# Performance work log

Hardware: AMD Instinct MI355X
Metric: run time of the kernel (lower is better)

Reference implementation:

```python
import jax, jax.numpy as jnp
import numpy as np

N_NODES = 100000
N_EDGES = 1600000


def spmm(edge_index, edge_vals, x, n_nodes):
    # adj @ x with adj in COO form: out[dst] += val * x[src]
    src = edge_index[0]
    dst = edge_index[1]
    gathered = x[src] * edge_vals[:, None]  # [E, F]
    return jax.ops.segment_sum(gathered, dst, num_segments=n_nodes)


def setup_inputs() -> dict:
    key = jax.random.key(0)
    ks = jax.random.split(key, 8)
    x = jax.random.normal(ks[0], (N_NODES, 512), dtype=jnp.float32)
    edge_index = jax.random.randint(ks[1], (2, N_EDGES), 0, N_NODES, dtype=jnp.int64)
    edge_vals = jax.random.uniform(ks[2], (N_EDGES,), dtype=jnp.float32)
    # xavier-uniform style weights, zero biases (as in initialize_weights)
    def xavier(k, fan_in, fan_out):
        lim = float(np.sqrt(6.0 / (fan_in + fan_out)))
        return jax.random.uniform(k, (fan_in, fan_out), minval=-lim, maxval=lim, dtype=jnp.float32)
    W1 = xavier(ks[3], 512, 128)
    b1 = jnp.zeros((128,), jnp.float32)
    W2 = xavier(ks[4], 128, 64)
    b2 = jnp.zeros((64,), jnp.float32)
    W3 = xavier(ks[5], 64, 16)
    b3 = jnp.zeros((16,), jnp.float32)
    return {"x": x, "edge_index": edge_index, "edge_vals": edge_vals,
            "W1": W1, "b1": b1, "W2": W2, "b2": b2, "W3": W3, "b3": b3}


def reference(x, edge_index, edge_vals, W1, b1, W2, b2, W3, b3):
    n = x.shape[0]
    h = jax.nn.relu(spmm(edge_index, edge_vals, x @ W1 + b1, n))
    h = jax.nn.relu(spmm(edge_index, edge_vals, h @ W2 + b2, n))
    logits = spmm(edge_index, edge_vals, h @ W3 + b3, n)
    logp = jax.nn.log_softmax(logits, axis=1)
    return jnp.argmax(logp, axis=1)
```

## Files before the change

### kernel.cpp

```cpp
#include <hip/hip_runtime.h>

typedef _Float16 half8 __attribute__((ext_vector_type(8)));
typedef float floatx4 __attribute__((ext_vector_type(4)));

__device__ __forceinline__ void g2lds16(const void* g, void* l) {
    __builtin_amdgcn_global_load_lds(
        (const __attribute__((address_space(1))) void*)(unsigned long long)g,
        (__attribute__((address_space(3))) void*)(unsigned int)(unsigned long long)l,
        16, 0, 0);
}


__global__ __launch_bounds__(256) void hist_kernel(const int* __restrict__ dst,
                                                   int* __restrict__ count, int E) {
    int e = blockIdx.x * 256 + threadIdx.x;
    if (e < E) atomicAdd(&count[dst[e]], 1);
}

__global__ __launch_bounds__(1024) void scan_a(const int* __restrict__ count,
                                               int* __restrict__ incl,
                                               int* __restrict__ bsum, int N) {
    __shared__ int s[1024];
    int tid = threadIdx.x;
    int i = blockIdx.x * 1024 + tid;
    int v = (i < N) ? count[i] : 0;
    s[tid] = v;
    __syncthreads();
    for (int off = 1; off < 1024; off <<= 1) {
        int t = (tid >= off) ? s[tid - off] : 0;
        __syncthreads();
        s[tid] += t;
        __syncthreads();
    }
    if (i < N) incl[i] = s[tid];
    if (tid == 1023) bsum[blockIdx.x] = s[1023];
}

__global__ void scan_b(const int* __restrict__ bsum, int* __restrict__ boff, int NB) {
    if (threadIdx.x == 0 && blockIdx.x == 0) {
        int run = 0;
        for (int b = 0; b < NB; ++b) { int c = bsum[b]; boff[b] = run; run += c; }
    }
}

__global__ __launch_bounds__(1024) void scan_c(const int* __restrict__ count,
                                               const int* __restrict__ incl,
                                               const int* __restrict__ boff,
                                               int* __restrict__ rowptr,
                                               int* __restrict__ cursor, int N) {
    int i = blockIdx.x * 1024 + threadIdx.x;
    if (i < N) {
        int excl = incl[i] - count[i] + boff[blockIdx.x];
        rowptr[i] = excl;
        cursor[i] = excl;
        if (i == N - 1) rowptr[N] = incl[i] + boff[blockIdx.x];
    }
}

__global__ __launch_bounds__(256) void scatter_kernel(const int* __restrict__ src,
                                                      const int* __restrict__ dst,
                                                      const float* __restrict__ val,
                                                      int* __restrict__ cursor,
                                                      int* __restrict__ ssrc,
                                                      float* __restrict__ sval, int E) {
    int e = blockIdx.x * 256 + threadIdx.x;
    if (e < E) {
        int d = dst[e];
        int pos = atomicAdd(&cursor[d], 1);
        ssrc[pos] = src[e];
        sval[pos] = val[e];
    }
}


__global__ __launch_bounds__(256) void prep_w1(const float* __restrict__ W1,
                                               _Float16* __restrict__ Whi,
                                               _Float16* __restrict__ Wlo) {
    int tid = blockIdx.x * 256 + threadIdx.x;
    int n = tid >> 9;
    int k = tid & 511;
    float w = W1[(size_t)k * 128 + n];
    _Float16 h = (_Float16)w;
    Whi[tid] = h;
    Wlo[tid] = (_Float16)(w - (float)h);
}

__global__ __launch_bounds__(256) void prep_w2(const float* __restrict__ W2,
                                               _Float16* __restrict__ Whi,
                                               _Float16* __restrict__ Wlo) {
    int tid = blockIdx.x * 256 + threadIdx.x;
    int n = tid >> 7;
    int k = tid & 127;
    float w = W2[(size_t)k * 64 + n];
    _Float16 h = (_Float16)w;
    Whi[tid] = h;
    Wlo[tid] = (_Float16)(w - (float)h);
}

__device__ __forceinline__ void split8(float4 f0, float4 f1, half8& h, half8& l) {
    float f[8] = {f0.x, f0.y, f0.z, f0.w, f1.x, f1.y, f1.z, f1.w};
#pragma unroll
    for (int j = 0; j < 8; ++j) {
        _Float16 hi = (_Float16)f[j];
        h[j] = hi;
        l[j] = (_Float16)(f[j] - (float)hi);
    }
}


__global__ __launch_bounds__(256) void gemm1_mfma(const float* __restrict__ X,
                                                  const _Float16* __restrict__ Whi,
                                                  const _Float16* __restrict__ Wlo,
                                                  const float* __restrict__ bias,
                                                  float* __restrict__ out, int M) {
    __shared__ char smem[2 * 16384];
    int t = threadIdx.x;
    int w = t >> 6;
    int lane = t & 63;
    int quad = lane >> 4;
    int l16 = lane & 15;
    int bm = blockIdx.x * 128;
    int m0 = bm + w * 32;

    int ra0 = min(m0 + l16, M - 1);
    int ra1 = min(m0 + 16 + l16, M - 1);
    const float* a0p = X + (size_t)ra0 * 512 + quad * 8;
    const float* a1p = X + (size_t)ra1 * 512 + quad * 8;

    int chunk0 = w * 4;
    const _Float16* gsrc[4];
#pragma unroll
    for (int c = 0; c < 4; ++c) {
        int idx = (chunk0 + c) * 1024 + lane * 16;
        int sec = idx >> 13;
        int row = (idx & 8191) >> 6;
        int kch = (idx >> 4) & 3;
        gsrc[c] = (sec ? Wlo : Whi) + (size_t)row * 512 + kch * 8;
    }
#pragma unroll
    for (int c = 0; c < 4; ++c)
        g2lds16(gsrc[c], smem + (chunk0 + c) * 1024);

    floatx4 acc[2][8];
#pragma unroll
    for (int mt = 0; mt < 2; ++mt)
#pragma unroll
        for (int nt = 0; nt < 8; ++nt) acc[mt][nt] = (floatx4){0.f, 0.f, 0.f, 0.f};

    for (int i = 0; i < 16; ++i) {
        int k0 = i * 32;
        __syncthreads();
        float4 af00 = *(const float4*)(a0p + k0);
        float4 af01 = *(const float4*)(a0p + k0 + 4);
        float4 af10 = *(const float4*)(a1p + k0);
        float4 af11 = *(const float4*)(a1p + k0 + 4);
        if (i < 15) {
            char* nbuf = smem + ((i + 1) & 1) * 16384;
#pragma unroll
            for (int c = 0; c < 4; ++c)
                g2lds16(gsrc[c] + k0 + 32, nbuf + (chunk0 + c) * 1024);
        }
        const char* buf = smem + (i & 1) * 16384;
        half8 bh[8], bl[8];
#pragma unroll
        for (int nt = 0; nt < 8; ++nt) {
            int off = (nt * 16 + l16) * 64 + quad * 16;
            bh[nt] = *(const half8*)(buf + off);
            bl[nt] = *(const half8*)(buf + 8192 + off);
        }
        half8 ah0, al0, ah1, al1;
        split8(af00, af01, ah0, al0);
        split8(af10, af11, ah1, al1);
#pragma unroll
        for (int nt = 0; nt < 8; ++nt) {
            acc[0][nt] = __builtin_amdgcn_mfma_f32_16x16x32_f16(ah0, bh[nt], acc[0][nt], 0, 0, 0);
            acc[1][nt] = __builtin_amdgcn_mfma_f32_16x16x32_f16(ah1, bh[nt], acc[1][nt], 0, 0, 0);
            acc[0][nt] = __builtin_amdgcn_mfma_f32_16x16x32_f16(ah0, bl[nt], acc[0][nt], 0, 0, 0);
            acc[1][nt] = __builtin_amdgcn_mfma_f32_16x16x32_f16(ah1, bl[nt], acc[1][nt], 0, 0, 0);
            acc[0][nt] = __builtin_amdgcn_mfma_f32_16x16x32_f16(al0, bh[nt], acc[0][nt], 0, 0, 0);
            acc[1][nt] = __builtin_amdgcn_mfma_f32_16x16x32_f16(al1, bh[nt], acc[1][nt], 0, 0, 0);
        }
    }

#pragma unroll
    for (int nt = 0; nt < 8; ++nt) {
        int col = nt * 16 + l16;
        float bv = bias[col];
#pragma unroll
        for (int mt = 0; mt < 2; ++mt)
#pragma unroll
            for (int r = 0; r < 4; ++r) {
                int row = m0 + mt * 16 + quad * 4 + r;
                if (row < M) out[(size_t)row * 128 + col] = acc[mt][nt][r] + bv;
            }
    }
}


__global__ __launch_bounds__(256) void gemm2_mfma(const float* __restrict__ H,
                                                  const _Float16* __restrict__ Whi,
                                                  const _Float16* __restrict__ Wlo,
                                                  const float* __restrict__ bias,
                                                  float* __restrict__ out, int M) {
    __shared__ char smem[2 * 64 * 320];
    int t = threadIdx.x;
#pragma unroll
    for (int i = 0; i < 4; ++i) {
        int gidx = i * 256 + t;
        int row = gidx >> 4, col = gidx & 15;
        *(float4*)(smem + row * 320 + col * 16) = ((const float4*)Whi)[gidx];
        *(float4*)(smem + 20480 + row * 320 + col * 16) = ((const float4*)Wlo)[gidx];
    }
    __syncthreads();

    int w = t >> 6;
    int lane = t & 63;
    int quad = lane >> 4;
    int l16 = lane & 15;
    int m0 = blockIdx.x * 128 + w * 32;
    int ra0 = min(m0 + l16, M - 1);
    int ra1 = min(m0 + 16 + l16, M - 1);
    const float* a0p = H + (size_t)ra0 * 128 + quad * 8;
    const float* a1p = H + (size_t)ra1 * 128 + quad * 8;

    floatx4 acc[2][4];
#pragma unroll
    for (int mt = 0; mt < 2; ++mt)
#pragma unroll
        for (int nt = 0; nt < 4; ++nt) acc[mt][nt] = (floatx4){0.f, 0.f, 0.f, 0.f};

#pragma unroll
    for (int k0 = 0; k0 < 128; k0 += 32) {
        float4 af00 = *(const float4*)(a0p + k0);
        float4 af01 = *(const float4*)(a0p + k0 + 4);
        float4 af10 = *(const float4*)(a1p + k0);
        float4 af11 = *(const float4*)(a1p + k0 + 4);
        af00.x = fmaxf(af00.x, 0.f); af00.y = fmaxf(af00.y, 0.f);
        af00.z = fmaxf(af00.z, 0.f); af00.w = fmaxf(af00.w, 0.f);
        af01.x = fmaxf(af01.x, 0.f); af01.y = fmaxf(af01.y, 0.f);
        af01.z = fmaxf(af01.z, 0.f); af01.w = fmaxf(af01.w, 0.f);
        af10.x = fmaxf(af10.x, 0.f); af10.y = fmaxf(af10.y, 0.f);
        af10.z = fmaxf(af10.z, 0.f); af10.w = fmaxf(af10.w, 0.f);
        af11.x = fmaxf(af11.x, 0.f); af11.y = fmaxf(af11.y, 0.f);
        af11.z = fmaxf(af11.z, 0.f); af11.w = fmaxf(af11.w, 0.f);
        half8 bh[4], bl[4];
#pragma unroll
        for (int nt = 0; nt < 4; ++nt) {
            int off = (nt * 16 + l16) * 320 + k0 * 2 + quad * 16;
            bh[nt] = *(const half8*)(smem + off);
            bl[nt] = *(const half8*)(smem + 20480 + off);
        }
        half8 ah0, al0, ah1, al1;
        split8(af00, af01, ah0, al0);
        split8(af10, af11, ah1, al1);
#pragma unroll
        for (int nt = 0; nt < 4; ++nt) {
            acc[0][nt] = __builtin_amdgcn_mfma_f32_16x16x32_f16(ah0, bh[nt], acc[0][nt], 0, 0, 0);
            acc[1][nt] = __builtin_amdgcn_mfma_f32_16x16x32_f16(ah1, bh[nt], acc[1][nt], 0, 0, 0);
            acc[0][nt] = __builtin_amdgcn_mfma_f32_16x16x32_f16(ah0, bl[nt], acc[0][nt], 0, 0, 0);
            acc[1][nt] = __builtin_amdgcn_mfma_f32_16x16x32_f16(ah1, bl[nt], acc[1][nt], 0, 0, 0);
            acc[0][nt] = __builtin_amdgcn_mfma_f32_16x16x32_f16(al0, bh[nt], acc[0][nt], 0, 0, 0);
            acc[1][nt] = __builtin_amdgcn_mfma_f32_16x16x32_f16(al1, bh[nt], acc[1][nt], 0, 0, 0);
        }
    }

#pragma unroll
    for (int nt = 0; nt < 4; ++nt) {
        int col = nt * 16 + l16;
        float bv = bias[col];
#pragma unroll
        for (int mt = 0; mt < 2; ++mt)
#pragma unroll
            for (int r = 0; r < 4; ++r) {
                int row = m0 + mt * 16 + quad * 4 + r;
                if (row < M) out[(size_t)row * 64 + col] = acc[mt][nt][r] + bv;
            }
    }
}


__global__ __launch_bounds__(256) void gemm3(const float* __restrict__ H,
                                             const float* __restrict__ W,
                                             const float* __restrict__ bias,
                                             float* __restrict__ out, int M) {
    __shared__ float Ws[64 * 16];
    __shared__ float Xs[32 * 68];
    int t = threadIdx.x;
    int m0 = blockIdx.x * 32;
    ((float4*)Ws)[t] = ((const float4*)W)[t];
#pragma unroll
    for (int i = 0; i < 2; i++) {
        int idx = t + i * 256;
        int gi = idx * 4;
        int row = gi >> 6, col = gi & 63;
        float4 v = make_float4(0.f, 0.f, 0.f, 0.f);
        if (m0 + row < M) v = *(const float4*)(H + (size_t)(m0 + row) * 64 + col);
        v.x = fmaxf(v.x, 0.f); v.y = fmaxf(v.y, 0.f);
        v.z = fmaxf(v.z, 0.f); v.w = fmaxf(v.w, 0.f);
        *(float4*)&Xs[row * 68 + col] = v;
    }
    __syncthreads();
    int node = t >> 3;
    int j = t & 7;
    float a0 = 0.f, a1 = 0.f;
#pragma unroll 8
    for (int k = 0; k < 64; ++k) {
        float xv = Xs[node * 68 + k];
        a0 += xv * Ws[k * 16 + j * 2];
        a1 += xv * Ws[k * 16 + j * 2 + 1];
    }
    int row = m0 + node;
    if (row < M) {
        a0 += bias[j * 2];
        a1 += bias[j * 2 + 1];
        float2 r = make_float2(a0, a1);
        *(float2*)(out + (size_t)row * 16 + j * 2) = r;
    }
}


__global__ __launch_bounds__(256) void spmm128(const int* __restrict__ rowptr,
                                               const int* __restrict__ ssrc,
                                               const float* __restrict__ sval,
                                               const float* __restrict__ T,
                                               float* __restrict__ H, int N) {
    int lane = threadIdx.x & 63;
    int node = __builtin_amdgcn_readfirstlane(blockIdx.x * 4 + (threadIdx.x >> 6));
    if (node >= N) return;
    int beg = rowptr[node], end = rowptr[node + 1];
    float a0 = 0.f, a1 = 0.f;
    int i = beg;
    int n4 = beg + ((end - beg) & ~3);
    for (; i < n4; i += 4) {
        int s0 = ssrc[i], s1 = ssrc[i + 1], s2 = ssrc[i + 2], s3 = ssrc[i + 3];
        float v0 = sval[i], v1 = sval[i + 1], v2 = sval[i + 2], v3 = sval[i + 3];
        const float* p0 = T + (size_t)s0 * 128;
        const float* p1 = T + (size_t)s1 * 128;
        const float* p2 = T + (size_t)s2 * 128;
        const float* p3 = T + (size_t)s3 * 128;
        float x0 = p0[lane], y0 = p0[lane + 64];
        float x1 = p1[lane], y1 = p1[lane + 64];
        float x2 = p2[lane], y2 = p2[lane + 64];
        float x3 = p3[lane], y3 = p3[lane + 64];
        a0 += v0 * x0; a1 += v0 * y0;
        a0 += v1 * x1; a1 += v1 * y1;
        a0 += v2 * x2; a1 += v2 * y2;
        a0 += v3 * x3; a1 += v3 * y3;
    }
    for (; i < end; ++i) {
        int s = ssrc[i];
        float v = sval[i];
        const float* p = T + (size_t)s * 128;
        a0 += v * p[lane];
        a1 += v * p[lane + 64];
    }
    float* o = H + (size_t)node * 128;
    o[lane] = a0;
    o[lane + 64] = a1;
}

__global__ __launch_bounds__(256) void spmm64(const int* __restrict__ rowptr,
                                              const int* __restrict__ ssrc,
                                              const float* __restrict__ sval,
                                              const float* __restrict__ T,
                                              float* __restrict__ H, int N) {
    int lane = threadIdx.x & 63;
    int node = __builtin_amdgcn_readfirstlane(blockIdx.x * 4 + (threadIdx.x >> 6));
    if (node >= N) return;
    int beg = rowptr[node], end = rowptr[node + 1];
    float a = 0.f;
    int i = beg;
    int n4 = beg + ((end - beg) & ~3);
    for (; i < n4; i += 4) {
        int s0 = ssrc[i], s1 = ssrc[i + 1], s2 = ssrc[i + 2], s3 = ssrc[i + 3];
        float v0 = sval[i], v1 = sval[i + 1], v2 = sval[i + 2], v3 = sval[i + 3];
        float x0 = T[(size_t)s0 * 64 + lane];
        float x1 = T[(size_t)s1 * 64 + lane];
        float x2 = T[(size_t)s2 * 64 + lane];
        float x3 = T[(size_t)s3 * 64 + lane];
        a += v0 * x0; a += v1 * x1; a += v2 * x2; a += v3 * x3;
    }
    for (; i < end; ++i) a += sval[i] * T[(size_t)ssrc[i] * 64 + lane];
    H[(size_t)node * 64 + lane] = a;
}

__global__ __launch_bounds__(256) void spmm_argmax(const int* __restrict__ rowptr,
                                                   const int* __restrict__ ssrc,
                                                   const float* __restrict__ sval,
                                                   const float* __restrict__ T,
                                                   int* __restrict__ out, int N) {
    int lane = threadIdx.x & 63;
    int wave = threadIdx.x >> 6;
    int sub = lane >> 4;
    int fl = lane & 15;
    int node = blockIdx.x * 16 + wave * 4 + sub;
    float acc = 0.f;
    if (node < N) {
        int beg = rowptr[node], end = rowptr[node + 1];
        int i = beg;
        int n4 = beg + ((end - beg) & ~3);
        for (; i < n4; i += 4) {
            int s0 = ssrc[i], s1 = ssrc[i + 1], s2 = ssrc[i + 2], s3 = ssrc[i + 3];
            float v0 = sval[i], v1 = sval[i + 1], v2 = sval[i + 2], v3 = sval[i + 3];
            float x0 = T[(size_t)s0 * 16 + fl];
            float x1 = T[(size_t)s1 * 16 + fl];
            float x2 = T[(size_t)s2 * 16 + fl];
            float x3 = T[(size_t)s3 * 16 + fl];
            acc += v0 * x0; acc += v1 * x1; acc += v2 * x2; acc += v3 * x3;
        }
        for (; i < end; ++i) acc += sval[i] * T[(size_t)ssrc[i] * 16 + fl];
    }
    float bv = acc;
    int bi = fl;
#pragma unroll
    for (int off = 8; off >= 1; off >>= 1) {
        float ov = __shfl_xor(bv, off, 64);
        int oi = __shfl_xor(bi, off, 64);
        if (ov > bv || (ov == bv && oi < bi)) { bv = ov; bi = oi; }
    }
    if (node < N && fl == 0) out[node] = bi;
}


extern "C" void kernel_launch(void* const* d_in, const int* in_sizes, int n_in,
                              void* d_out, int out_size, void* d_ws, size_t ws_size,
                              hipStream_t stream) {
    const float* x  = (const float*)d_in[0];
    const int*   ei = (const int*)d_in[1];
    const float* ev = (const float*)d_in[2];
    const float* W1 = (const float*)d_in[3];
    const float* b1 = (const float*)d_in[4];
    const float* W2 = (const float*)d_in[5];
    const float* b2 = (const float*)d_in[6];
    const float* W3 = (const float*)d_in[7];
    const float* b3 = (const float*)d_in[8];
    int* out = (int*)d_out;

    int M = in_sizes[0] / 512;
    int E = in_sizes[2];
    const int* src = ei;
    const int* dst = ei + E;

    char* ws = (char*)d_ws;
    size_t off = 0;
    auto alloc = [&](size_t bytes) {
        size_t o = off;
        off += (bytes + 255) & ~(size_t)255;
        return o;
    };
    float*    tA     = (float*)(ws + alloc((size_t)M * 128 * 4));
    float*    hB     = (float*)(ws + alloc((size_t)M * 128 * 4));
    int*      ssrc   = (int*)  (ws + alloc((size_t)E * 4));
    float*    sval   = (float*)(ws + alloc((size_t)E * 4));
    int*      rowptr = (int*)  (ws + alloc((size_t)(M + 1) * 4));
    int*      cursor = (int*)  (ws + alloc((size_t)M * 4));
    int*      count  = (int*)  (ws + alloc((size_t)M * 4));
    int*      incl   = (int*)  (ws + alloc((size_t)M * 4));
    int*      bsum   = (int*)  (ws + alloc(4096));
    int*      boff   = (int*)  (ws + alloc(4096));
    _Float16* w1hi   = (_Float16*)(ws + alloc(512 * 128 * 2));
    _Float16* w1lo   = (_Float16*)(ws + alloc(512 * 128 * 2));
    _Float16* w2hi   = (_Float16*)(ws + alloc(128 * 64 * 2));
    _Float16* w2lo   = (_Float16*)(ws + alloc(128 * 64 * 2));

    hipMemsetAsync(count, 0, (size_t)M * 4, stream);
    prep_w1<<<256, 256, 0, stream>>>(W1, w1hi, w1lo);
    prep_w2<<<32, 256, 0, stream>>>(W2, w2hi, w2lo);
    hist_kernel<<<(E + 255) / 256, 256, 0, stream>>>(dst, count, E);
    int NB = (M + 1023) / 1024;
    scan_a<<<NB, 1024, 0, stream>>>(count, incl, bsum, M);
    scan_b<<<1, 64, 0, stream>>>(bsum, boff, NB);
    scan_c<<<NB, 1024, 0, stream>>>(count, incl, boff, rowptr, cursor, M);
    scatter_kernel<<<(E + 255) / 256, 256, 0, stream>>>(src, dst, ev, cursor, ssrc, sval, E);

    gemm1_mfma<<<(M + 127) / 128, 256, 0, stream>>>(x, w1hi, w1lo, b1, tA, M);
    spmm128<<<(M + 3) / 4, 256, 0, stream>>>(rowptr, ssrc, sval, tA, hB, M);
    gemm2_mfma<<<(M + 127) / 128, 256, 0, stream>>>(hB, w2hi, w2lo, b2, tA, M);
    spmm64<<<(M + 3) / 4, 256, 0, stream>>>(rowptr, ssrc, sval, tA, hB, M);
    gemm3<<<(M + 31) / 32, 256, 0, stream>>>(hB, W3, b3, tA, M);
    spmm_argmax<<<(M + 15) / 16, 256, 0, stream>>>(rowptr, ssrc, sval, tA, out, M);
}
```

Baseline: 753.8 us.

## Interleave CSR src/val, parallelize block-offset scan, prefetch A fragments in gemm1

Packs each edge's source index and weight into a single int2 array so the three SpMM kernels issue one 8-byte load per edge instead of two separate 4-byte streams. Replaces the single-thread serial block-offset scan with a 1024-thread shared-memory parallel scan. In gemm1 the next K-step's X fragments are loaded one iteration ahead (register double-buffering) to hide global latency behind MFMAs, at the cost of extra registers.

```diff
diff --git a/kernel.cpp b/kernel.cpp
--- a/kernel.cpp
+++ b/kernel.cpp
@@ -36,11 +36,20 @@
     if (tid == 1023) bsum[blockIdx.x] = s[1023];
 }
 
-__global__ void scan_b(const int* __restrict__ bsum, int* __restrict__ boff, int NB) {
-    if (threadIdx.x == 0 && blockIdx.x == 0) {
-        int run = 0;
-        for (int b = 0; b < NB; ++b) { int c = bsum[b]; boff[b] = run; run += c; }
-    }
+__global__ __launch_bounds__(1024) void scan_b(const int* __restrict__ bsum,
+                                               int* __restrict__ boff, int NB) {
+    __shared__ int s[1024];
+    int tid = threadIdx.x;
+    int v = (tid < NB) ? bsum[tid] : 0;
+    s[tid] = v;
+    __syncthreads();
+    for (int off = 1; off < 1024; off <<= 1) {
+        int t = (tid >= off) ? s[tid - off] : 0;
+        __syncthreads();
+        s[tid] += t;
+        __syncthreads();
+    }
+    if (tid < NB) boff[tid] = s[tid] - v;
 }
 
 __global__ __launch_bounds__(1024) void scan_c(const int* __restrict__ count,
@@ -61,14 +70,15 @@
                                                       const int* __restrict__ dst,
                                                       const float* __restrict__ val,
                                                       int* __restrict__ cursor,
-                                                      int* __restrict__ ssrc,
-                                                      float* __restrict__ sval, int E) {
+                                                      int2* __restrict__ ssv, int E) {
     int e = blockIdx.x * 256 + threadIdx.x;
     if (e < E) {
         int d = dst[e];
         int pos = atomicAdd(&cursor[d], 1);
-        ssrc[pos] = src[e];
-        sval[pos] = val[e];
+        int2 p;
+        p.x = src[e];
+        p.y = __float_as_int(val[e]);
+        ssv[pos] = p;
     }
 }
 
@@ -140,6 +150,10 @@
 #pragma unroll
     for (int c = 0; c < 4; ++c)
         g2lds16(gsrc[c], smem + (chunk0 + c) * 1024);
+    float4 af00 = *(const float4*)(a0p);
+    float4 af01 = *(const float4*)(a0p + 4);
+    float4 af10 = *(const float4*)(a1p);
+    float4 af11 = *(const float4*)(a1p + 4);
 
     floatx4 acc[2][8];
 #pragma unroll
@@ -150,15 +164,18 @@
     for (int i = 0; i < 16; ++i) {
         int k0 = i * 32;
         __syncthreads();
-        float4 af00 = *(const float4*)(a0p + k0);
-        float4 af01 = *(const float4*)(a0p + k0 + 4);
-        float4 af10 = *(const float4*)(a1p + k0);
-        float4 af11 = *(const float4*)(a1p + k0 + 4);
         if (i < 15) {
             char* nbuf = smem + ((i + 1) & 1) * 16384;
 #pragma unroll
             for (int c = 0; c < 4; ++c)
                 g2lds16(gsrc[c] + k0 + 32, nbuf + (chunk0 + c) * 1024);
+        }
+        float4 nf00 = af00, nf01 = af01, nf10 = af10, nf11 = af11;
+        if (i < 15) {
+            nf00 = *(const float4*)(a0p + k0 + 32);
+            nf01 = *(const float4*)(a0p + k0 + 36);
+            nf10 = *(const float4*)(a1p + k0 + 32);
+            nf11 = *(const float4*)(a1p + k0 + 36);
         }
         const char* buf = smem + (i & 1) * 16384;
         half8 bh[8], bl[8];
@@ -180,6 +197,7 @@
             acc[0][nt] = __builtin_amdgcn_mfma_f32_16x16x32_f16(al0, bh[nt], acc[0][nt], 0, 0, 0);
             acc[1][nt] = __builtin_amdgcn_mfma_f32_16x16x32_f16(al1, bh[nt], acc[1][nt], 0, 0, 0);
         }
+        af00 = nf00; af01 = nf01; af10 = nf10; af11 = nf11;
     }
 
 #pragma unroll
@@ -320,8 +338,7 @@
 
 
 __global__ __launch_bounds__(256) void spmm128(const int* __restrict__ rowptr,
-                                               const int* __restrict__ ssrc,
-                                               const float* __restrict__ sval,
+                                               const int2* __restrict__ ssv,
                                                const float* __restrict__ T,
                                                float* __restrict__ H, int N) {
     int lane = threadIdx.x & 63;
@@ -332,25 +349,26 @@
     int i = beg;
     int n4 = beg + ((end - beg) & ~3);
     for (; i < n4; i += 4) {
-        int s0 = ssrc[i], s1 = ssrc[i + 1], s2 = ssrc[i + 2], s3 = ssrc[i + 3];
-        float v0 = sval[i], v1 = sval[i + 1], v2 = sval[i + 2], v3 = sval[i + 3];
-        const float* p0 = T + (size_t)s0 * 128;
-        const float* p1 = T + (size_t)s1 * 128;
-        const float* p2 = T + (size_t)s2 * 128;
-        const float* p3 = T + (size_t)s3 * 128;
+        int2 e0 = ssv[i], e1 = ssv[i + 1], e2 = ssv[i + 2], e3 = ssv[i + 3];
+        const float* p0 = T + (size_t)e0.x * 128;
+        const float* p1 = T + (size_t)e1.x * 128;
+        const float* p2 = T + (size_t)e2.x * 128;
+        const float* p3 = T + (size_t)e3.x * 128;
         float x0 = p0[lane], y0 = p0[lane + 64];
         float x1 = p1[lane], y1 = p1[lane + 64];
         float x2 = p2[lane], y2 = p2[lane + 64];
         float x3 = p3[lane], y3 = p3[lane + 64];
+        float v0 = __int_as_float(e0.y), v1 = __int_as_float(e1.y);
+        float v2 = __int_as_float(e2.y), v3 = __int_as_float(e3.y);
         a0 += v0 * x0; a1 += v0 * y0;
         a0 += v1 * x1; a1 += v1 * y1;
         a0 += v2 * x2; a1 += v2 * y2;
         a0 += v3 * x3; a1 += v3 * y3;
     }
     for (; i < end; ++i) {
-        int s = ssrc[i];
-        float v = sval[i];
-        const float* p = T + (size_t)s * 128;
+        int2 e = ssv[i];
+        float v = __int_as_float(e.y);
+        const float* p = T + (size_t)e.x * 128;
         a0 += v * p[lane];
         a1 += v * p[lane + 64];
     }
@@ -360,8 +378,7 @@
 }
 
 __global__ __launch_bounds__(256) void spmm64(const int* __restrict__ rowptr,
-                                              const int* __restrict__ ssrc,
-                                              const float* __restrict__ sval,
+                                              const int2* __restrict__ ssv,
                                               const float* __restrict__ T,
                                               float* __restrict__ H, int N) {
     int lane = threadIdx.x & 63;
@@ -372,21 +389,25 @@
     int i = beg;
     int n4 = beg + ((end - beg) & ~3);
     for (; i < n4; i += 4) {
-        int s0 = ssrc[i], s1 = ssrc[i + 1], s2 = ssrc[i + 2], s3 = ssrc[i + 3];
-        float v0 = sval[i], v1 = sval[i + 1], v2 = sval[i + 2], v3 = sval[i + 3];
-        float x0 = T[(size_t)s0 * 64 + lane];
-        float x1 = T[(size_t)s1 * 64 + lane];
-        float x2 = T[(size_t)s2 * 64 + lane];
-        float x3 = T[(size_t)s3 * 64 + lane];
-        a += v0 * x0; a += v1 * x1; a += v2 * x2; a += v3 * x3;
-    }
-    for (; i < end; ++i) a += sval[i] * T[(size_t)ssrc[i] * 64 + lane];
+        int2 e0 = ssv[i], e1 = ssv[i + 1], e2 = ssv[i + 2], e3 = ssv[i + 3];
+        float x0 = T[(size_t)e0.x * 64 + lane];
+        float x1 = T[(size_t)e1.x * 64 + lane];
+        float x2 = T[(size_t)e2.x * 64 + lane];
+        float x3 = T[(size_t)e3.x * 64 + lane];
+        a += __int_as_float(e0.y) * x0;
+        a += __int_as_float(e1.y) * x1;
+        a += __int_as_float(e2.y) * x2;
+        a += __int_as_float(e3.y) * x3;
+    }
+    for (; i < end; ++i) {
+        int2 e = ssv[i];
+        a += __int_as_float(e.y) * T[(size_t)e.x * 64 + lane];
+    }
     H[(size_t)node * 64 + lane] = a;
 }
 
 __global__ __launch_bounds__(256) void spmm_argmax(const int* __restrict__ rowptr,
-                                                   const int* __restrict__ ssrc,
-                                                   const float* __restrict__ sval,
+                                                   const int2* __restrict__ ssv,
                                                    const float* __restrict__ T,
                                                    int* __restrict__ out, int N) {
     int lane = threadIdx.x & 63;
@@ -400,15 +421,20 @@
         int i = beg;
         int n4 = beg + ((end - beg) & ~3);
         for (; i < n4; i += 4) {
-            int s0 = ssrc[i], s1 = ssrc[i + 1], s2 = ssrc[i + 2], s3 = ssrc[i + 3];
-            float v0 = sval[i], v1 = sval[i + 1], v2 = sval[i + 2], v3 = sval[i + 3];
-            float x0 = T[(size_t)s0 * 16 + fl];
-            float x1 = T[(size_t)s1 * 16 + fl];
-            float x2 = T[(size_t)s2 * 16 + fl];
-            float x3 = T[(size_t)s3 * 16 + fl];
-            acc += v0 * x0; acc += v1 * x1; acc += v2 * x2; acc += v3 * x3;
-        }
-        for (; i < end; ++i) acc += sval[i] * T[(size_t)ssrc[i] * 16 + fl];
+            int2 e0 = ssv[i], e1 = ssv[i + 1], e2 = ssv[i + 2], e3 = ssv[i + 3];
+            float x0 = T[(size_t)e0.x * 16 + fl];
+            float x1 = T[(size_t)e1.x * 16 + fl];
+            float x2 = T[(size_t)e2.x * 16 + fl];
+            float x3 = T[(size_t)e3.x * 16 + fl];
+            acc += __int_as_float(e0.y) * x0;
+            acc += __int_as_float(e1.y) * x1;
+            acc += __int_as_float(e2.y) * x2;
+            acc += __int_as_float(e3.y) * x3;
+        }
+        for (; i < end; ++i) {
+            int2 e = ssv[i];
+            acc += __int_as_float(e.y) * T[(size_t)e.x * 16 + fl];
+        }
     }
     float bv = acc;
     int bi = fl;
@@ -450,8 +476,7 @@
     };
     float*    tA     = (float*)(ws + alloc((size_t)M * 128 * 4));
     float*    hB     = (float*)(ws + alloc((size_t)M * 128 * 4));
-    int*      ssrc   = (int*)  (ws + alloc((size_t)E * 4));
-    float*    sval   = (float*)(ws + alloc((size_t)E * 4));
+    int2*     ssv    = (int2*) (ws + alloc((size_t)E * 8));
     int*      rowptr = (int*)  (ws + alloc((size_t)(M + 1) * 4));
     int*      cursor = (int*)  (ws + alloc((size_t)M * 4));
     int*      count  = (int*)  (ws + alloc((size_t)M * 4));
@@ -469,14 +494,14 @@
     hist_kernel<<<(E + 255) / 256, 256, 0, stream>>>(dst, count, E);
     int NB = (M + 1023) / 1024;
     scan_a<<<NB, 1024, 0, stream>>>(count, incl, bsum, M);
-    scan_b<<<1, 64, 0, stream>>>(bsum, boff, NB);
+    scan_b<<<1, 1024, 0, stream>>>(bsum, boff, NB);
     scan_c<<<NB, 1024, 0, stream>>>(count, incl, boff, rowptr, cursor, M);
-    scatter_kernel<<<(E + 255) / 256, 256, 0, stream>>>(src, dst, ev, cursor, ssrc, sval, E);
+    scatter_kernel<<<(E + 255) / 256, 256, 0, stream>>>(src, dst, ev, cursor, ssv, E);
 
     gemm1_mfma<<<(M + 127) / 128, 256, 0, stream>>>(x, w1hi, w1lo, b1, tA, M);
-    spmm128<<<(M + 3) / 4, 256, 0, stream>>>(rowptr, ssrc, sval, tA, hB, M);
+    spmm128<<<(M + 3) / 4, 256, 0, stream>>>(rowptr, ssv, tA, hB, M);
     gemm2_mfma<<<(M + 127) / 128, 256, 0, stream>>>(hB, w2hi, w2lo, b2, tA, M);
-    spmm64<<<(M + 3) / 4, 256, 0, stream>>>(rowptr, ssrc, sval, tA, hB, M);
+    spmm64<<<(M + 3) / 4, 256, 0, stream>>>(rowptr, ssv, tA, hB, M);
     gemm3<<<(M + 31) / 32, 256, 0, stream>>>(hB, W3, b3, tA, M);
-    spmm_argmax<<<(M + 15) / 16, 256, 0, stream>>>(rowptr, ssrc, sval, tA, out, M);
-}
+    spmm_argmax<<<(M + 15) / 16, 256, 0, stream>>>(rowptr, ssv, tA, out, M);
+}
```

After: 755.3 us. About the same (+0.2%).
